# Performance work log

Measured on AMD Instinct MI355X. Metric: run time of the kernel, lower is better.

Reference implementation:

```python
import jax, jax.numpy as jnp
import numpy as np

MUL = 128            # shared multiplicity (channels)
D_IN = 9             # 0e(1)+1o(3)+2e(5)
DIMS_OUT = (1, 3, 5) # output irrep dims: 0e,1o,2e
P3, P2, P1 = 6, 3, 1 # CG path counts per output irrep for degrees 3,2,1
NUM_ELEMENTS = 10
BATCH = 2048


def _make_u(rng, shape, keep=0.15):
    # Sparse fixed Clebsch-Gordan-like basis tensor (constant buffer).
    vals = rng.standard_normal(shape).astype(np.float32)
    mask = rng.random(shape) < keep
    return jnp.asarray(np.where(mask, vals, 0.0).astype(np.float32))


def setup_inputs() -> dict:
    key = jax.random.key(0)
    kx, ki, kw = jax.random.split(key, 3)
    inp = {
        'x': jax.random.normal(kx, (BATCH, MUL, D_IN), dtype=jnp.float32),
        'indices': jax.random.randint(ki, (BATCH,), 0, NUM_ELEMENTS, dtype=jnp.int32),
        'weight': jax.random.normal(kw, (NUM_ELEMENTS, len(DIMS_OUT) * (P3 + P2 + P1), MUL), dtype=jnp.float32) * 0.1,
    }
    rng = np.random.default_rng(0)
    for j, o in enumerate(DIMS_OUT):
        inp[f'U3_{j}'] = _make_u(rng, (o, D_IN, D_IN, D_IN, P3))
        inp[f'U2_{j}'] = _make_u(rng, (o, D_IN, D_IN, P2))
        inp[f'U1_{j}'] = _make_u(rng, (o, D_IN, P1))
    return inp


def _symmetric_contraction(x, indices, weight, us):
    # x: (b, mul, d_in); indices: (b,); weight: (E, total_paths, mul)
    # us: list of (U3, U2, U1) per output irrep.
    b = x.shape[0]
    outs, off = [], 0
    for U3, U2, U1 in us:
        w3 = weight[:, off:off + P3][indices]; off += P3  # (b, P3, mul)
        w2 = weight[:, off:off + P2][indices]; off += P2
        w1 = weight[:, off:off + P1][indices]; off += P1
        # degree-3 term: contract last CG input axis with x, paths with weights
        out = jnp.einsum('oijlk,bkc,bcl->bcoij', U3, w3, x)   # (b,c,o,9,9)
        c2 = jnp.einsum('oijk,bkc->bcoij', U2, w2) + out
        out = jnp.einsum('bcoij,bcj->bcoi', c2, x)            # (b,c,o,9)
        c1 = jnp.einsum('oik,bkc->bcoi', U1, w1) + out
        out = jnp.einsum('bcoi,bci->bco', c1, x)              # (b,c,o)
        outs.append(out.reshape(b, -1))                       # mul_ir layout block
    return jnp.concatenate(outs, axis=-1)                     # (b, mul*sum(dims_out))


def reference(x, indices, weight, U3_0, U2_0, U1_0, U3_1, U2_1, U1_1, U3_2, U2_2, U1_2):
    us = [(U3_0, U2_0, U1_0), (U3_1, U2_1, U1_1), (U3_2, U2_2, U1_2)]
    return _symmetric_contraction(x, indices, weight, us)
```

## Files before the change

kernel.cpp:

```cpp
#include <hip/hip_runtime.h>

#define BATCH 2048
#define NTRI 165
#define NPAIR 45
#define NSTEP 14
#define UCHUNKS (NSTEP * 3 * 64)

typedef __attribute__((ext_vector_type(8))) short s16x8;
typedef __attribute__((ext_vector_type(16))) float f32x16;
typedef __attribute__((ext_vector_type(4))) int i32x4;

struct TriTab { unsigned char a[NTRI], b[NTRI], c[NTRI]; };
constexpr TriTab make_tri() {
  TriTab t{}; int q = 0;
  for (int a = 0; a < 9; a++) for (int b = a; b < 9; b++) for (int c = b; c < 9; c++) {
    t.a[q] = (unsigned char)a; t.b[q] = (unsigned char)b; t.c[q] = (unsigned char)c; q++;
  }
  return t;
}
constexpr TriTab TRI = make_tri();

struct PairTab { unsigned char a[NPAIR], b[NPAIR]; };
constexpr PairTab make_pair() {
  PairTab t{}; int q = 0;
  for (int a = 0; a < 9; a++) for (int b = a; b < 9; b++) {
    t.a[q] = (unsigned char)a; t.b[q] = (unsigned char)b; q++;
  }
  return t;
}
constexpr PairTab PAIR = make_pair();

__global__ void prep_kernel(const float* __restrict__ U30, const float* __restrict__ U20, const float* __restrict__ U10,
                            const float* __restrict__ U31, const float* __restrict__ U21, const float* __restrict__ U11,
                            const float* __restrict__ U32, const float* __restrict__ U22, const float* __restrict__ U12,
                            unsigned short* __restrict__ wsB) {
  int t = blockIdx.x * blockDim.x + threadIdx.x;
  if (t >= UCHUNKS * 8) return;
  int j = t & 7;
  int lane = (t >> 3) & 63;
  int cf = t >> 9;
  int s = cf / 3, ct = cf % 3;
  int n = ct * 32 + (lane & 31);
  int k = s * 16 + (lane >> 5) * 8 + j;
  const float* U3[3] = {U30, U31, U32};
  const float* U2[3] = {U20, U21, U22};
  const float* U1[3] = {U10, U11, U12};
  float val = 0.f;
  if (n < 54) {
    if (k < NTRI) {
      int o = n / 6, j3 = n % 6;
      int ir = (o > 0) + (o > 3); int lo = o - (ir == 1 ? 1 : (ir == 2 ? 4 : 0));
      int a = TRI.a[k], b = TRI.b[k], cc = TRI.c[k];
      int pm[6][3] = {{a,b,cc},{a,cc,b},{b,a,cc},{b,cc,a},{cc,a,b},{cc,b,a}};
      for (int p = 0; p < 6; p++) {
        bool dup = false;
        for (int rr = 0; rr < p; rr++)
          if (pm[rr][0] == pm[p][0] && pm[rr][1] == pm[p][1] && pm[rr][2] == pm[p][2]) dup = true;
        if (!dup) val += U3[ir][(((lo * 9 + pm[p][0]) * 9 + pm[p][1]) * 9 + pm[p][2]) * 6 + j3];
      }
    }
  } else if (n < 81) {
    if (k >= NTRI && k < NTRI + NPAIR) {
      int o = (n - 54) / 3, j2 = (n - 54) % 3;
      int ir = (o > 0) + (o > 3); int lo = o - (ir == 1 ? 1 : (ir == 2 ? 4 : 0));
      int p = k - NTRI;
      int a = PAIR.a[p], b = PAIR.b[p];
      val = U2[ir][((lo * 9 + a) * 9 + b) * 3 + j2];
      if (a != b) val += U2[ir][((lo * 9 + b) * 9 + a) * 3 + j2];
    }
  } else if (n < 90) {
    if (k >= 210 && k < 219) {
      int o = n - 81;
      int ir = (o > 0) + (o > 3); int lo = o - (ir == 1 ? 1 : (ir == 2 ? 4 : 0));
      val = U1[ir][lo * 9 + (k - 210)];
    }
  }
  unsigned u = __float_as_uint(val);
  unsigned r = (u + 0x7FFFu + ((u >> 16) & 1u)) >> 16;
  wsB[t] = (unsigned short)r;
}

template<int K>
__device__ __forceinline__ float mono(const float* xx) {
  if constexpr (K < NTRI)              return xx[TRI.a[K]] * xx[TRI.b[K]] * xx[TRI.c[K]];
  else if constexpr (K < NTRI + NPAIR) return xx[PAIR.a[K - NTRI]] * xx[PAIR.b[K - NTRI]];
  else if constexpr (K < 219)          return xx[K - 210];
  else                                 return 0.f;
}

template<int S>
__device__ __forceinline__ void pipe(const float* xx, const int g2, const i32x4* Uf, const int l,
                                     f32x16& acc0, f32x16& acc1, f32x16& acc2,
                                     i32x4 c0, i32x4 c1, i32x4 c2,
                                     i32x4 n0, i32x4 n1, i32x4 n2) {
  i32x4 f0{}, f1{}, f2{};
  if constexpr (S + 2 < NSTEP) {
    f0 = Uf[((S + 2) * 3 + 0) * 64 + l];
    f1 = Uf[((S + 2) * 3 + 1) * 64 + l];
    f2 = Uf[((S + 2) * 3 + 2) * 64 + l];
  }
  unsigned q0, q1, q2, q3;
  {
    float lo = g2 ? mono<S*16+8>(xx)  : mono<S*16+0>(xx);
    float hi = g2 ? mono<S*16+9>(xx)  : mono<S*16+1>(xx);
    asm("v_cvt_pk_bf16_f32 %0, %1, %2" : "=v"(q0) : "v"(lo), "v"(hi));
  }
  {
    float lo = g2 ? mono<S*16+10>(xx) : mono<S*16+2>(xx);
    float hi = g2 ? mono<S*16+11>(xx) : mono<S*16+3>(xx);
    asm("v_cvt_pk_bf16_f32 %0, %1, %2" : "=v"(q1) : "v"(lo), "v"(hi));
  }
  {
    float lo = g2 ? mono<S*16+12>(xx) : mono<S*16+4>(xx);
    float hi = g2 ? mono<S*16+13>(xx) : mono<S*16+5>(xx);
    asm("v_cvt_pk_bf16_f32 %0, %1, %2" : "=v"(q2) : "v"(lo), "v"(hi));
  }
  {
    float lo = g2 ? mono<S*16+14>(xx) : mono<S*16+6>(xx);
    float hi = g2 ? mono<S*16+15>(xx) : mono<S*16+7>(xx);
    asm("v_cvt_pk_bf16_f32 %0, %1, %2" : "=v"(q3) : "v"(lo), "v"(hi));
  }
  i32x4 bi;
  bi[0] = (int)q0; bi[1] = (int)q1; bi[2] = (int)q2; bi[3] = (int)q3;
  s16x8 bf = __builtin_bit_cast(s16x8, bi);
  acc0 = __builtin_amdgcn_mfma_f32_32x32x16_bf16(__builtin_bit_cast(s16x8, c0), bf, acc0, 0, 0, 0);
  acc1 = __builtin_amdgcn_mfma_f32_32x32x16_bf16(__builtin_bit_cast(s16x8, c1), bf, acc1, 0, 0, 0);
  acc2 = __builtin_amdgcn_mfma_f32_32x32x16_bf16(__builtin_bit_cast(s16x8, c2), bf, acc2, 0, 0, 0);
  if constexpr (S + 1 < NSTEP)
    pipe<S + 1>(xx, g2, Uf, l, acc0, acc1, acc2, n0, n1, n2, f0, f1, f2);
}

#define ACCV(ct) ((ct) == 0 ? acc0 : (ct) == 1 ? acc1 : acc2)

__global__ __launch_bounds__(256) void symcon_mfma(
    const float* __restrict__ x, const int* __restrict__ indices,
    const float* __restrict__ w, const unsigned short* __restrict__ wsB,
    float* __restrict__ out)
{
  const int tid = threadIdx.x;
  const int wave = tid >> 6;
  const int l = tid & 63;
  const int l5 = l & 31;
  const int g2 = l >> 5;

  const int b = blockIdx.x;
  const int c = wave * 32 + l5;

  const float* xp = x + ((size_t)b * 128 + c) * 9;
  float xx[9];
#pragma unroll
  for (int i = 0; i < 9; i++) xx[i] = xp[i];

  const int e = indices[b];

  f32x16 acc0, acc1, acc2;
#pragma unroll
  for (int i = 0; i < 16; i++) { acc0[i] = 0.f; acc1[i] = 0.f; acc2[i] = 0.f; }

  const i32x4* Uf = (const i32x4*)wsB;
  i32x4 p0 = Uf[0 * 64 + l], p1 = Uf[1 * 64 + l], p2 = Uf[2 * 64 + l];
  i32x4 r0 = Uf[3 * 64 + l], r1 = Uf[4 * 64 + l], r2 = Uf[5 * 64 + l];
  pipe<0>(xx, g2, Uf, l, acc0, acc1, acc2, p0, p1, p2, r0, r1, r2);

  const float* wbase = w + (size_t)e * 30 * 128 + c;
  float wv[30];
#pragma unroll
  for (int p = 0; p < 30; p++) wv[p] = wbase[p * 128];

  float* orow = out + (size_t)b * 1152;
#pragma unroll
  for (int o = 0; o < 9; o++) {
    const int ir = (o > 0) + (o > 3);
    float p0f = 0.f, p1f = 0.f;
#pragma unroll
    for (int k3 = 0; k3 < 6; k3++) {
      const int n = 6 * o + k3;
      const int nl = n & 31, ct = n >> 5;
      const int reg = (nl & 3) + 4 * (nl >> 3);
      const float cf = wv[ir * 10 + k3];
      if (((nl >> 2) & 1) == 0) p0f = fmaf(ACCV(ct)[reg], cf, p0f);
      else                      p1f = fmaf(ACCV(ct)[reg], cf, p1f);
    }
#pragma unroll
    for (int k2 = 0; k2 < 3; k2++) {
      const int n = 54 + 3 * o + k2;
      const int nl = n & 31, ct = n >> 5;
      const int reg = (nl & 3) + 4 * (nl >> 3);
      const float cf = wv[ir * 10 + 6 + k2];
      if (((nl >> 2) & 1) == 0) p0f = fmaf(ACCV(ct)[reg], cf, p0f);
      else                      p1f = fmaf(ACCV(ct)[reg], cf, p1f);
    }
    {
      const int n = 81 + o;
      const int nl = n & 31, ct = n >> 5;
      const int reg = (nl & 3) + 4 * (nl >> 3);
      const float cf = wv[ir * 10 + 9];
      if (((nl >> 2) & 1) == 0) p0f = fmaf(ACCV(ct)[reg], cf, p0f);
      else                      p1f = fmaf(ACCV(ct)[reg], cf, p1f);
    }
    float p = g2 ? p1f : p0f;
    p += __shfl_xor(p, 32);
    const int col = (o == 0) ? c : (o < 4 ? 128 + 3 * c + (o - 1) : 512 + 5 * c + (o - 4));
    const bool mine = (o < 5) ? (g2 == 0) : (g2 == 1);
    if (mine) orow[col] = p;
  }
}

extern "C" void kernel_launch(void* const* d_in, const int* in_sizes, int n_in,
                              void* d_out, int out_size, void* d_ws, size_t ws_size,
                              hipStream_t stream) {
  const float* x   = (const float*)d_in[0];
  const int*   idx = (const int*)d_in[1];
  const float* w   = (const float*)d_in[2];
  const float* U30 = (const float*)d_in[3];
  const float* U20 = (const float*)d_in[4];
  const float* U10 = (const float*)d_in[5];
  const float* U31 = (const float*)d_in[6];
  const float* U21 = (const float*)d_in[7];
  const float* U11 = (const float*)d_in[8];
  const float* U32 = (const float*)d_in[9];
  const float* U22 = (const float*)d_in[10];
  const float* U12 = (const float*)d_in[11];
  unsigned short* wsB = (unsigned short*)d_ws;
  float* out = (float*)d_out;

  prep_kernel<<<(UCHUNKS * 8 + 255) / 256, 256, 0, stream>>>(U30, U20, U10, U31, U21, U11, U32, U22, U12, wsB);
  symcon_mfma<<<BATCH, 256, 0, stream>>>(x, idx, w, wsB, out);
}
```

Measured before the change: 36.04 us.

## Process two batch rows per block to reuse U fragments across MFMAs

Each block now handles two batch elements. Every U-tensor fragment loaded from the workspace feeds two MFMAs, one per row, and the grid is halved. This cuts global loads of U per batch element and lengthens the independent MFMA chains to hide latency. In exchange it doubles the accumulator registers (six 16-wide accumulators), which may lower occupancy, and halves the number of blocks.

```diff
diff --git a/kernel.cpp b/kernel.cpp
--- a/kernel.cpp
+++ b/kernel.cpp
@@ -89,8 +89,38 @@
 }
 
 template<int S>
-__device__ __forceinline__ void pipe(const float* xx, const int g2, const i32x4* Uf, const int l,
-                                     f32x16& acc0, f32x16& acc1, f32x16& acc2,
+__device__ __forceinline__ s16x8 makeB(const float* xx, const int g2) {
+  unsigned q0, q1, q2, q3;
+  {
+    float lo = g2 ? mono<S*16+8>(xx)  : mono<S*16+0>(xx);
+    float hi = g2 ? mono<S*16+9>(xx)  : mono<S*16+1>(xx);
+    asm("v_cvt_pk_bf16_f32 %0, %1, %2" : "=v"(q0) : "v"(lo), "v"(hi));
+  }
+  {
+    float lo = g2 ? mono<S*16+10>(xx) : mono<S*16+2>(xx);
+    float hi = g2 ? mono<S*16+11>(xx) : mono<S*16+3>(xx);
+    asm("v_cvt_pk_bf16_f32 %0, %1, %2" : "=v"(q1) : "v"(lo), "v"(hi));
+  }
+  {
+    float lo = g2 ? mono<S*16+12>(xx) : mono<S*16+4>(xx);
+    float hi = g2 ? mono<S*16+13>(xx) : mono<S*16+5>(xx);
+    asm("v_cvt_pk_bf16_f32 %0, %1, %2" : "=v"(q2) : "v"(lo), "v"(hi));
+  }
+  {
+    float lo = g2 ? mono<S*16+14>(xx) : mono<S*16+6>(xx);
+    float hi = g2 ? mono<S*16+15>(xx) : mono<S*16+7>(xx);
+    asm("v_cvt_pk_bf16_f32 %0, %1, %2" : "=v"(q3) : "v"(lo), "v"(hi));
+  }
+  i32x4 bi;
+  bi[0] = (int)q0; bi[1] = (int)q1; bi[2] = (int)q2; bi[3] = (int)q3;
+  return __builtin_bit_cast(s16x8, bi);
+}
+
+template<int S>
+__device__ __forceinline__ void pipe(const float* xx0, const float* xx1, const int g2,
+                                     const i32x4* Uf, const int l,
+                                     f32x16& a00, f32x16& a01, f32x16& a02,
+                                     f32x16& a10, f32x16& a11, f32x16& a12,
                                      i32x4 c0, i32x4 c1, i32x4 c2,
                                      i32x4 n0, i32x4 n1, i32x4 n2) {
   i32x4 f0{}, f1{}, f2{};
@@ -99,38 +129,20 @@
     f1 = Uf[((S + 2) * 3 + 1) * 64 + l];
     f2 = Uf[((S + 2) * 3 + 2) * 64 + l];
   }
-  unsigned q0, q1, q2, q3;
-  {
-    float lo = g2 ? mono<S*16+8>(xx)  : mono<S*16+0>(xx);
-    float hi = g2 ? mono<S*16+9>(xx)  : mono<S*16+1>(xx);
-    asm("v_cvt_pk_bf16_f32 %0, %1, %2" : "=v"(q0) : "v"(lo), "v"(hi));
-  }
-  {
-    float lo = g2 ? mono<S*16+10>(xx) : mono<S*16+2>(xx);
-    float hi = g2 ? mono<S*16+11>(xx) : mono<S*16+3>(xx);
-    asm("v_cvt_pk_bf16_f32 %0, %1, %2" : "=v"(q1) : "v"(lo), "v"(hi));
-  }
-  {
-    float lo = g2 ? mono<S*16+12>(xx) : mono<S*16+4>(xx);
-    float hi = g2 ? mono<S*16+13>(xx) : mono<S*16+5>(xx);
-    asm("v_cvt_pk_bf16_f32 %0, %1, %2" : "=v"(q2) : "v"(lo), "v"(hi));
-  }
-  {
-    float lo = g2 ? mono<S*16+14>(xx) : mono<S*16+6>(xx);
-    float hi = g2 ? mono<S*16+15>(xx) : mono<S*16+7>(xx);
-    asm("v_cvt_pk_bf16_f32 %0, %1, %2" : "=v"(q3) : "v"(lo), "v"(hi));
-  }
-  i32x4 bi;
-  bi[0] = (int)q0; bi[1] = (int)q1; bi[2] = (int)q2; bi[3] = (int)q3;
-  s16x8 bf = __builtin_bit_cast(s16x8, bi);
-  acc0 = __builtin_amdgcn_mfma_f32_32x32x16_bf16(__builtin_bit_cast(s16x8, c0), bf, acc0, 0, 0, 0);
-  acc1 = __builtin_amdgcn_mfma_f32_32x32x16_bf16(__builtin_bit_cast(s16x8, c1), bf, acc1, 0, 0, 0);
-  acc2 = __builtin_amdgcn_mfma_f32_32x32x16_bf16(__builtin_bit_cast(s16x8, c2), bf, acc2, 0, 0, 0);
+  s16x8 bf0 = makeB<S>(xx0, g2);
+  s16x8 bf1 = makeB<S>(xx1, g2);
+  s16x8 u0 = __builtin_bit_cast(s16x8, c0);
+  s16x8 u1 = __builtin_bit_cast(s16x8, c1);
+  s16x8 u2 = __builtin_bit_cast(s16x8, c2);
+  a00 = __builtin_amdgcn_mfma_f32_32x32x16_bf16(u0, bf0, a00, 0, 0, 0);
+  a10 = __builtin_amdgcn_mfma_f32_32x32x16_bf16(u0, bf1, a10, 0, 0, 0);
+  a01 = __builtin_amdgcn_mfma_f32_32x32x16_bf16(u1, bf0, a01, 0, 0, 0);
+  a11 = __builtin_amdgcn_mfma_f32_32x32x16_bf16(u1, bf1, a11, 0, 0, 0);
+  a02 = __builtin_amdgcn_mfma_f32_32x32x16_bf16(u2, bf0, a02, 0, 0, 0);
+  a12 = __builtin_amdgcn_mfma_f32_32x32x16_bf16(u2, bf1, a12, 0, 0, 0);
   if constexpr (S + 1 < NSTEP)
-    pipe<S + 1>(xx, g2, Uf, l, acc0, acc1, acc2, n0, n1, n2, f0, f1, f2);
-}
-
-#define ACCV(ct) ((ct) == 0 ? acc0 : (ct) == 1 ? acc1 : acc2)
+    pipe<S + 1>(xx0, xx1, g2, Uf, l, a00, a01, a02, a10, a11, a12, n0, n1, n2, f0, f1, f2);
+}
 
 __global__ __launch_bounds__(256) void symcon_mfma(
     const float* __restrict__ x, const int* __restrict__ indices,
@@ -143,66 +155,85 @@
   const int l5 = l & 31;
   const int g2 = l >> 5;
 
-  const int b = blockIdx.x;
+  const int b0 = blockIdx.x * 2;
+  const int b1 = b0 + 1;
   const int c = wave * 32 + l5;
 
-  const float* xp = x + ((size_t)b * 128 + c) * 9;
-  float xx[9];
-#pragma unroll
-  for (int i = 0; i < 9; i++) xx[i] = xp[i];
-
-  const int e = indices[b];
-
-  f32x16 acc0, acc1, acc2;
-#pragma unroll
-  for (int i = 0; i < 16; i++) { acc0[i] = 0.f; acc1[i] = 0.f; acc2[i] = 0.f; }
+  float xx0[9], xx1[9];
+  {
+    const float* xp0 = x + ((size_t)b0 * 128 + c) * 9;
+    const float* xp1 = x + ((size_t)b1 * 128 + c) * 9;
+#pragma unroll
+    for (int i = 0; i < 9; i++) { xx0[i] = xp0[i]; xx1[i] = xp1[i]; }
+  }
+
+  const int e0 = indices[b0];
+  const int e1 = indices[b1];
+
+  f32x16 a00, a01, a02, a10, a11, a12;
+#pragma unroll
+  for (int i = 0; i < 16; i++) {
+    a00[i] = 0.f; a01[i] = 0.f; a02[i] = 0.f;
+    a10[i] = 0.f; a11[i] = 0.f; a12[i] = 0.f;
+  }
 
   const i32x4* Uf = (const i32x4*)wsB;
   i32x4 p0 = Uf[0 * 64 + l], p1 = Uf[1 * 64 + l], p2 = Uf[2 * 64 + l];
   i32x4 r0 = Uf[3 * 64 + l], r1 = Uf[4 * 64 + l], r2 = Uf[5 * 64 + l];
-  pipe<0>(xx, g2, Uf, l, acc0, acc1, acc2, p0, p1, p2, r0, r1, r2);
-
-  const float* wbase = w + (size_t)e * 30 * 128 + c;
-  float wv[30];
-#pragma unroll
-  for (int p = 0; p < 30; p++) wv[p] = wbase[p * 128];
-
-  float* orow = out + (size_t)b * 1152;
-#pragma unroll
-  for (int o = 0; o < 9; o++) {
-    const int ir = (o > 0) + (o > 3);
-    float p0f = 0.f, p1f = 0.f;
-#pragma unroll
-    for (int k3 = 0; k3 < 6; k3++) {
-      const int n = 6 * o + k3;
-      const int nl = n & 31, ct = n >> 5;
-      const int reg = (nl & 3) + 4 * (nl >> 3);
-      const float cf = wv[ir * 10 + k3];
-      if (((nl >> 2) & 1) == 0) p0f = fmaf(ACCV(ct)[reg], cf, p0f);
-      else                      p1f = fmaf(ACCV(ct)[reg], cf, p1f);
-    }
-#pragma unroll
-    for (int k2 = 0; k2 < 3; k2++) {
-      const int n = 54 + 3 * o + k2;
-      const int nl = n & 31, ct = n >> 5;
-      const int reg = (nl & 3) + 4 * (nl >> 3);
-      const float cf = wv[ir * 10 + 6 + k2];
-      if (((nl >> 2) & 1) == 0) p0f = fmaf(ACCV(ct)[reg], cf, p0f);
-      else                      p1f = fmaf(ACCV(ct)[reg], cf, p1f);
-    }
-    {
-      const int n = 81 + o;
-      const int nl = n & 31, ct = n >> 5;
-      const int reg = (nl & 3) + 4 * (nl >> 3);
-      const float cf = wv[ir * 10 + 9];
-      if (((nl >> 2) & 1) == 0) p0f = fmaf(ACCV(ct)[reg], cf, p0f);
-      else                      p1f = fmaf(ACCV(ct)[reg], cf, p1f);
-    }
-    float p = g2 ? p1f : p0f;
-    p += __shfl_xor(p, 32);
-    const int col = (o == 0) ? c : (o < 4 ? 128 + 3 * c + (o - 1) : 512 + 5 * c + (o - 4));
-    const bool mine = (o < 5) ? (g2 == 0) : (g2 == 1);
-    if (mine) orow[col] = p;
+  pipe<0>(xx0, xx1, g2, Uf, l, a00, a01, a02, a10, a11, a12, p0, p1, p2, r0, r1, r2);
+
+#pragma unroll
+  for (int row = 0; row < 2; row++) {
+    const int b = row ? b1 : b0;
+    const int e = row ? e1 : e0;
+    const float* wbase = w + (size_t)e * 30 * 128 + c;
+    float wv[30];
+#pragma unroll
+    for (int p = 0; p < 30; p++) wv[p] = wbase[p * 128];
+
+    float* orow = out + (size_t)b * 1152;
+#pragma unroll
+    for (int o = 0; o < 9; o++) {
+      const int ir = (o > 0) + (o > 3);
+      float p0f = 0.f, p1f = 0.f;
+#pragma unroll
+      for (int k3 = 0; k3 < 6; k3++) {
+        const int n = 6 * o + k3;
+        const int nl = n & 31, ct = n >> 5;
+        const int reg = (nl & 3) + 4 * (nl >> 3);
+        const float av = row ? (ct == 0 ? a10[reg] : ct == 1 ? a11[reg] : a12[reg])
+                             : (ct == 0 ? a00[reg] : ct == 1 ? a01[reg] : a02[reg]);
+        const float cf = wv[ir * 10 + k3];
+        if (((nl >> 2) & 1) == 0) p0f = fmaf(av, cf, p0f);
+        else                      p1f = fmaf(av, cf, p1f);
+      }
+#pragma unroll
+      for (int k2 = 0; k2 < 3; k2++) {
+        const int n = 54 + 3 * o + k2;
+        const int nl = n & 31, ct = n >> 5;
+        const int reg = (nl & 3) + 4 * (nl >> 3);
+        const float av = row ? (ct == 0 ? a10[reg] : ct == 1 ? a11[reg] : a12[reg])
+                             : (ct == 0 ? a00[reg] : ct == 1 ? a01[reg] : a02[reg]);
+        const float cf = wv[ir * 10 + 6 + k2];
+        if (((nl >> 2) & 1) == 0) p0f = fmaf(av, cf, p0f);
+        else                      p1f = fmaf(av, cf, p1f);
+      }
+      {
+        const int n = 81 + o;
+        const int nl = n & 31, ct = n >> 5;
+        const int reg = (nl & 3) + 4 * (nl >> 3);
+        const float av = row ? (ct == 0 ? a10[reg] : ct == 1 ? a11[reg] : a12[reg])
+                             : (ct == 0 ? a00[reg] : ct == 1 ? a01[reg] : a02[reg]);
+        const float cf = wv[ir * 10 + 9];
+        if (((nl >> 2) & 1) == 0) p0f = fmaf(av, cf, p0f);
+        else                      p1f = fmaf(av, cf, p1f);
+      }
+      float p = g2 ? p1f : p0f;
+      p += __shfl_xor(p, 32);
+      const int col = (o == 0) ? c : (o < 4 ? 128 + 3 * c + (o - 1) : 512 + 5 * c + (o - 4));
+      const bool mine = (o < 5) ? (g2 == 0) : (g2 == 1);
+      if (mine) orow[col] = p;
+    }
   }
 }
 
@@ -225,5 +256,5 @@
   float* out = (float*)d_out;
 
   prep_kernel<<<(UCHUNKS * 8 + 255) / 256, 256, 0, stream>>>(U30, U20, U10, U31, U21, U11, U32, U22, U12, wsB);
-  symcon_mfma<<<BATCH, 256, 0, stream>>>(x, idx, w, wsB, out);
-}
+  symcon_mfma<<<BATCH / 2, 256, 0, stream>>>(x, idx, w, wsB, out);
+}
```

Result: no change. 36.08 us (+0.1%).

## Reorder monomial slots to share pair products and prefetch weights mid-pipeline

Applied to the files above, without the earlier changes.

Reorders the K dimension so that degree-3 monomials sharing their first two factors land in the two lane halves of the same MFMA slot. Each lane then computes the shared pair product once and multiplies by a lane-selected third factor, which cuts the per-lane arithmetic and select work when building the B fragments. The prep kernel is rewritten to emit the symmetrised U values in the matching slot order. The per-channel weight loads are also moved into the pipeline at step 10, so their latency overlaps the remaining MFMAs, at the cost of more live registers during the pipeline.

```diff
diff --git a/kernel.cpp b/kernel.cpp
--- a/kernel.cpp
+++ b/kernel.cpp
@@ -1,34 +1,51 @@
 #include <hip/hip_runtime.h>
 
 #define BATCH 2048
-#define NTRI 165
-#define NPAIR 45
 #define NSTEP 14
+#define NSLOT 224
 #define UCHUNKS (NSTEP * 3 * 64)
 
 typedef __attribute__((ext_vector_type(8))) short s16x8;
 typedef __attribute__((ext_vector_type(16))) float f32x16;
 typedef __attribute__((ext_vector_type(4))) int i32x4;
 
-struct TriTab { unsigned char a[NTRI], b[NTRI], c[NTRI]; };
-constexpr TriTab make_tri() {
-  TriTab t{}; int q = 0;
+struct SlotTab { signed char ty[NSLOT], a[NSLOT], b[NSLOT], c[NSLOT]; };
+constexpr SlotTab make_slots() {
+  SlotTab st{};
+  for (int q = 0; q < NSLOT; q++) { st.ty[q] = 0; st.a[q] = 0; st.b[q] = 0; st.c[q] = 0; }
+  int ta[165], tb[165], tc[165]; int nt = 0;
   for (int a = 0; a < 9; a++) for (int b = a; b < 9; b++) for (int c = b; c < 9; c++) {
-    t.a[q] = (unsigned char)a; t.b[q] = (unsigned char)b; t.c[q] = (unsigned char)c; q++;
-  }
-  return t;
-}
-constexpr TriTab TRI = make_tri();
-
-struct PairTab { unsigned char a[NPAIR], b[NPAIR]; };
-constexpr PairTab make_pair() {
-  PairTab t{}; int q = 0;
-  for (int a = 0; a < 9; a++) for (int b = a; b < 9; b++) {
-    t.a[q] = (unsigned char)a; t.b[q] = (unsigned char)b; q++;
-  }
-  return t;
-}
-constexpr PairTab PAIR = make_pair();
+    ta[nt] = a; tb[nt] = b; tc[nt] = c; nt++;
+  }
+  int p0[83], p1[83]; int np = 0;
+  int sing[165]; int ns = 0;
+  {
+    int i = 0;
+    while (i < 165) {
+      if (i + 1 < 165 && ta[i] == ta[i + 1] && tb[i] == tb[i + 1]) { p0[np] = i; p1[np] = i + 1; np++; i += 2; }
+      else { sing[ns++] = i; i++; }
+    }
+  }
+  for (int j = 0; j < np; j++) {
+    int s = j / 8, t = j % 8;
+    int q0 = s * 16 + t, q1 = s * 16 + 8 + t;
+    st.ty[q0] = 3; st.a[q0] = (signed char)ta[p0[j]]; st.b[q0] = (signed char)tb[p0[j]]; st.c[q0] = (signed char)tc[p0[j]];
+    st.ty[q1] = 3; st.a[q1] = (signed char)ta[p1[j]]; st.b[q1] = (signed char)tb[p1[j]]; st.c[q1] = (signed char)tc[p1[j]];
+  }
+  int ity[84], ia[84], ib[84], ic[84]; int ni = 0;
+  for (int j = 0; j < ns; j++) { ity[ni] = 3; ia[ni] = ta[sing[j]]; ib[ni] = tb[sing[j]]; ic[ni] = tc[sing[j]]; ni++; }
+  for (int a = 0; a < 9; a++) for (int b = a; b < 9; b++) { ity[ni] = 2; ia[ni] = a; ib[ni] = b; ic[ni] = 0; ni++; }
+  for (int i = 0; i < 9; i++) { ity[ni] = 1; ia[ni] = i; ib[ni] = 0; ic[ni] = 0; ni++; }
+  while (ni < 84) { ity[ni] = 0; ia[ni] = 0; ib[ni] = 0; ic[ni] = 0; ni++; }
+  for (int j = 0; j < 84; j++) {
+    int pos = np + j / 2;
+    int s = pos / 8, t = pos % 8;
+    int q = s * 16 + (j % 2) * 8 + t;
+    st.ty[q] = (signed char)ity[j]; st.a[q] = (signed char)ia[j]; st.b[q] = (signed char)ib[j]; st.c[q] = (signed char)ic[j];
+  }
+  return st;
+}
+constexpr SlotTab SLOTS = make_slots();
 
 __global__ void prep_kernel(const float* __restrict__ U30, const float* __restrict__ U20, const float* __restrict__ U10,
                             const float* __restrict__ U31, const float* __restrict__ U21, const float* __restrict__ U11,
@@ -45,51 +62,73 @@
   const float* U3[3] = {U30, U31, U32};
   const float* U2[3] = {U20, U21, U22};
   const float* U1[3] = {U10, U11, U12};
+  const int ty = SLOTS.ty[k], a = SLOTS.a[k], b = SLOTS.b[k], cc = SLOTS.c[k];
   float val = 0.f;
-  if (n < 54) {
-    if (k < NTRI) {
-      int o = n / 6, j3 = n % 6;
-      int ir = (o > 0) + (o > 3); int lo = o - (ir == 1 ? 1 : (ir == 2 ? 4 : 0));
-      int a = TRI.a[k], b = TRI.b[k], cc = TRI.c[k];
-      int pm[6][3] = {{a,b,cc},{a,cc,b},{b,a,cc},{b,cc,a},{cc,a,b},{cc,b,a}};
-      for (int p = 0; p < 6; p++) {
-        bool dup = false;
-        for (int rr = 0; rr < p; rr++)
-          if (pm[rr][0] == pm[p][0] && pm[rr][1] == pm[p][1] && pm[rr][2] == pm[p][2]) dup = true;
-        if (!dup) val += U3[ir][(((lo * 9 + pm[p][0]) * 9 + pm[p][1]) * 9 + pm[p][2]) * 6 + j3];
-      }
-    }
-  } else if (n < 81) {
-    if (k >= NTRI && k < NTRI + NPAIR) {
-      int o = (n - 54) / 3, j2 = (n - 54) % 3;
-      int ir = (o > 0) + (o > 3); int lo = o - (ir == 1 ? 1 : (ir == 2 ? 4 : 0));
-      int p = k - NTRI;
-      int a = PAIR.a[p], b = PAIR.b[p];
-      val = U2[ir][((lo * 9 + a) * 9 + b) * 3 + j2];
-      if (a != b) val += U2[ir][((lo * 9 + b) * 9 + a) * 3 + j2];
-    }
-  } else if (n < 90) {
-    if (k >= 210 && k < 219) {
-      int o = n - 81;
-      int ir = (o > 0) + (o > 3); int lo = o - (ir == 1 ? 1 : (ir == 2 ? 4 : 0));
-      val = U1[ir][lo * 9 + (k - 210)];
-    }
+  if (ty == 3 && n < 54) {
+    int o = n / 6, j3 = n % 6;
+    int ir = (o > 0) + (o > 3); int lo = o - (ir == 1 ? 1 : (ir == 2 ? 4 : 0));
+    int pm[6][3] = {{a,b,cc},{a,cc,b},{b,a,cc},{b,cc,a},{cc,a,b},{cc,b,a}};
+    for (int p = 0; p < 6; p++) {
+      bool dup = false;
+      for (int rr = 0; rr < p; rr++)
+        if (pm[rr][0] == pm[p][0] && pm[rr][1] == pm[p][1] && pm[rr][2] == pm[p][2]) dup = true;
+      if (!dup) val += U3[ir][(((lo * 9 + pm[p][0]) * 9 + pm[p][1]) * 9 + pm[p][2]) * 6 + j3];
+    }
+  } else if (ty == 2 && n >= 54 && n < 81) {
+    int o = (n - 54) / 3, j2 = (n - 54) % 3;
+    int ir = (o > 0) + (o > 3); int lo = o - (ir == 1 ? 1 : (ir == 2 ? 4 : 0));
+    val = U2[ir][((lo * 9 + a) * 9 + b) * 3 + j2];
+    if (a != b) val += U2[ir][((lo * 9 + b) * 9 + a) * 3 + j2];
+  } else if (ty == 1 && n >= 81 && n < 90) {
+    int o = n - 81;
+    int ir = (o > 0) + (o > 3); int lo = o - (ir == 1 ? 1 : (ir == 2 ? 4 : 0));
+    val = U1[ir][lo * 9 + a];
   }
   unsigned u = __float_as_uint(val);
   unsigned r = (u + 0x7FFFu + ((u >> 16) & 1u)) >> 16;
   wsB[t] = (unsigned short)r;
 }
 
-template<int K>
-__device__ __forceinline__ float mono(const float* xx) {
-  if constexpr (K < NTRI)              return xx[TRI.a[K]] * xx[TRI.b[K]] * xx[TRI.c[K]];
-  else if constexpr (K < NTRI + NPAIR) return xx[PAIR.a[K - NTRI]] * xx[PAIR.b[K - NTRI]];
-  else if constexpr (K < 219)          return xx[K - 210];
+template<int Q>
+__device__ __forceinline__ float monoQ(const float* xx) {
+  if constexpr (SLOTS.ty[Q] == 3)      return xx[SLOTS.a[Q]] * xx[SLOTS.b[Q]] * xx[SLOTS.c[Q]];
+  else if constexpr (SLOTS.ty[Q] == 2) return xx[SLOTS.a[Q]] * xx[SLOTS.b[Q]];
+  else if constexpr (SLOTS.ty[Q] == 1) return xx[SLOTS.a[Q]];
   else                                 return 0.f;
+}
+
+template<int S, int T>
+__device__ __forceinline__ float slotval(const float* xx, const int g2) {
+  constexpr int Q0 = S * 16 + T, Q1 = S * 16 + 8 + T;
+  if constexpr (SLOTS.ty[Q0] == 3 && SLOTS.ty[Q1] == 3 &&
+                SLOTS.a[Q0] == SLOTS.a[Q1] && SLOTS.b[Q0] == SLOTS.b[Q1]) {
+    float P = xx[SLOTS.a[Q0]] * xx[SLOTS.b[Q0]];
+    float xc = g2 ? xx[SLOTS.c[Q1]] : xx[SLOTS.c[Q0]];
+    return P * xc;
+  } else {
+    return g2 ? monoQ<Q1>(xx) : monoQ<Q0>(xx);
+  }
+}
+
+template<int S>
+__device__ __forceinline__ s16x8 makeB(const float* xx, const int g2) {
+  unsigned q0, q1, q2, q3;
+  { float lo = slotval<S,0>(xx,g2), hi = slotval<S,1>(xx,g2);
+    asm("v_cvt_pk_bf16_f32 %0, %1, %2" : "=v"(q0) : "v"(lo), "v"(hi)); }
+  { float lo = slotval<S,2>(xx,g2), hi = slotval<S,3>(xx,g2);
+    asm("v_cvt_pk_bf16_f32 %0, %1, %2" : "=v"(q1) : "v"(lo), "v"(hi)); }
+  { float lo = slotval<S,4>(xx,g2), hi = slotval<S,5>(xx,g2);
+    asm("v_cvt_pk_bf16_f32 %0, %1, %2" : "=v"(q2) : "v"(lo), "v"(hi)); }
+  { float lo = slotval<S,6>(xx,g2), hi = slotval<S,7>(xx,g2);
+    asm("v_cvt_pk_bf16_f32 %0, %1, %2" : "=v"(q3) : "v"(lo), "v"(hi)); }
+  i32x4 bi;
+  bi[0] = (int)q0; bi[1] = (int)q1; bi[2] = (int)q2; bi[3] = (int)q3;
+  return __builtin_bit_cast(s16x8, bi);
 }
 
 template<int S>
 __device__ __forceinline__ void pipe(const float* xx, const int g2, const i32x4* Uf, const int l,
+                                     const float* wbase, float* wv,
                                      f32x16& acc0, f32x16& acc1, f32x16& acc2,
                                      i32x4 c0, i32x4 c1, i32x4 c2,
                                      i32x4 n0, i32x4 n1, i32x4 n2) {
@@ -99,35 +138,16 @@
     f1 = Uf[((S + 2) * 3 + 1) * 64 + l];
     f2 = Uf[((S + 2) * 3 + 2) * 64 + l];
   }
-  unsigned q0, q1, q2, q3;
-  {
-    float lo = g2 ? mono<S*16+8>(xx)  : mono<S*16+0>(xx);
-    float hi = g2 ? mono<S*16+9>(xx)  : mono<S*16+1>(xx);
-    asm("v_cvt_pk_bf16_f32 %0, %1, %2" : "=v"(q0) : "v"(lo), "v"(hi));
-  }
-  {
-    float lo = g2 ? mono<S*16+10>(xx) : mono<S*16+2>(xx);
-    float hi = g2 ? mono<S*16+11>(xx) : mono<S*16+3>(xx);
-    asm("v_cvt_pk_bf16_f32 %0, %1, %2" : "=v"(q1) : "v"(lo), "v"(hi));
-  }
-  {
-    float lo = g2 ? mono<S*16+12>(xx) : mono<S*16+4>(xx);
-    float hi = g2 ? mono<S*16+13>(xx) : mono<S*16+5>(xx);
-    asm("v_cvt_pk_bf16_f32 %0, %1, %2" : "=v"(q2) : "v"(lo), "v"(hi));
-  }
-  {
-    float lo = g2 ? mono<S*16+14>(xx) : mono<S*16+6>(xx);
-    float hi = g2 ? mono<S*16+15>(xx) : mono<S*16+7>(xx);
-    asm("v_cvt_pk_bf16_f32 %0, %1, %2" : "=v"(q3) : "v"(lo), "v"(hi));
-  }
-  i32x4 bi;
-  bi[0] = (int)q0; bi[1] = (int)q1; bi[2] = (int)q2; bi[3] = (int)q3;
-  s16x8 bf = __builtin_bit_cast(s16x8, bi);
+  if constexpr (S == 10) {
+#pragma unroll
+    for (int p = 0; p < 30; p++) wv[p] = wbase[p * 128];
+  }
+  s16x8 bf = makeB<S>(xx, g2);
   acc0 = __builtin_amdgcn_mfma_f32_32x32x16_bf16(__builtin_bit_cast(s16x8, c0), bf, acc0, 0, 0, 0);
   acc1 = __builtin_amdgcn_mfma_f32_32x32x16_bf16(__builtin_bit_cast(s16x8, c1), bf, acc1, 0, 0, 0);
   acc2 = __builtin_amdgcn_mfma_f32_32x32x16_bf16(__builtin_bit_cast(s16x8, c2), bf, acc2, 0, 0, 0);
   if constexpr (S + 1 < NSTEP)
-    pipe<S + 1>(xx, g2, Uf, l, acc0, acc1, acc2, n0, n1, n2, f0, f1, f2);
+    pipe<S + 1>(xx, g2, Uf, l, wbase, wv, acc0, acc1, acc2, n0, n1, n2, f0, f1, f2);
 }
 
 #define ACCV(ct) ((ct) == 0 ? acc0 : (ct) == 1 ? acc1 : acc2)
@@ -152,6 +172,8 @@
   for (int i = 0; i < 9; i++) xx[i] = xp[i];
 
   const int e = indices[b];
+  const float* wbase = w + (size_t)e * 30 * 128 + c;
+  float wv[30];
 
   f32x16 acc0, acc1, acc2;
 #pragma unroll
@@ -160,12 +182,7 @@
   const i32x4* Uf = (const i32x4*)wsB;
   i32x4 p0 = Uf[0 * 64 + l], p1 = Uf[1 * 64 + l], p2 = Uf[2 * 64 + l];
   i32x4 r0 = Uf[3 * 64 + l], r1 = Uf[4 * 64 + l], r2 = Uf[5 * 64 + l];
-  pipe<0>(xx, g2, Uf, l, acc0, acc1, acc2, p0, p1, p2, r0, r1, r2);
-
-  const float* wbase = w + (size_t)e * 30 * 128 + c;
-  float wv[30];
-#pragma unroll
-  for (int p = 0; p < 30; p++) wv[p] = wbase[p * 128];
+  pipe<0>(xx, g2, Uf, l, wbase, wv, acc0, acc1, acc2, p0, p1, p2, r0, r1, r2);
 
   float* orow = out + (size_t)b * 1152;
 #pragma unroll
```

Result: slower. 37.37 us (+3.7%).
